# Performance work log

Measured on AMD Instinct MI355X. Metric: run time of the kernel, lower is better.

## Reference

```python
import jax, jax.numpy as jnp
import numpy as np

N = 100000   # points
C = 256      # in_planes
K = 16       # nsample (idx holds 2*K neighbors)
L = 2        # num_mlplayer
NEG = 0.1    # LeakyReLU slope
EPS = 1e-5   # LayerNorm eps (torch default)

PARAM_KEYS = ['emb_w1','emb_g1','emb_b1','emb_w2','conv_w','pw_w1','pw_g1','pw_b1','pw_w2','pw_g2','pw_b2']


def layer_norm(x, g, b):
    m = x.mean(-1, keepdims=True)
    v = ((x - m) ** 2).mean(-1, keepdims=True)
    return (x - m) * jax.lax.rsqrt(v + EPS) * g + b


def calc_ppf(p, n, pg, ng):
    # standard 4-dim point-pair features: angle(n1,d), angle(n2,d), angle(n1,n2), ||d||
    d = pg - p[:, None, :]                                   # [N,2K,3]
    dist = jnp.linalg.norm(d, axis=-1, keepdims=True)
    def angle(a, b):
        cr = jnp.linalg.norm(jnp.cross(a, b), axis=-1, keepdims=True)
        dt = jnp.sum(a * b, axis=-1, keepdims=True)
        return jnp.arctan2(cr, dt)
    n1 = jnp.broadcast_to(n[:, None, :], pg.shape)
    return jnp.concatenate([angle(n1, d), angle(ng, d), angle(n1, ng), dist], -1)


def mlp_layer(p, x, idx, ppf, r, pr):
    # cart2sphere -> r-normalized radial distance, giving 4+1=5 embedding inputs
    d = p[idx] - p[:, None, :]                               # [N,K,3]
    sphere = jnp.linalg.norm(d, axis=-1, keepdims=True) / r  # [N,K,1]
    f5 = jnp.concatenate([ppf, sphere], -1)                  # [N,K,5]
    h = f5 @ pr['emb_w1']
    h = jax.nn.leaky_relu(layer_norm(h, pr['emb_g1'], pr['emb_b1']), NEG)
    pos = h @ pr['emb_w2']                                   # [N,K,C]
    g = x[idx] + pos                                         # gather + add
    # Partial_conv3 (split_cat): 1x1 conv (no bias) on first C//4 channels
    c4 = pr['conv_w'].shape[0]
    g1 = jnp.einsum('nkc,dc->nkd', g[..., :c4], pr['conv_w'])
    g = jnp.concatenate([g1, g[..., c4:]], -1)
    pooled = g.max(axis=1)                                   # max-pool over neighbors [N,C]
    h = pooled @ pr['pw_w1']
    h = jax.nn.leaky_relu(layer_norm(h, pr['pw_g1'], pr['pw_b1']), NEG)
    h = layer_norm(h @ pr['pw_w2'], pr['pw_g2'], pr['pw_b2'])
    return jax.nn.relu(h + x)                                # residual + relu


def setup_inputs():
    key = jax.random.key(0)
    ks = jax.random.split(key, 16)
    s = 0.02
    n = jax.random.normal(ks[2], (N, 3), jnp.float32)
    n = n / jnp.linalg.norm(n, axis=-1, keepdims=True)
    return {
        'p': jax.random.normal(ks[0], (N, 3), jnp.float32),
        'x': jax.random.normal(ks[1], (N, C), jnp.float32),
        'n': n,
        'idx': jax.random.randint(ks[3], (N, 2 * K), 0, N, jnp.int32),
        'r': jnp.ones((1,), jnp.float32),
        'emb_w1': jax.random.normal(ks[4], (L, 5, C), jnp.float32) * s,
        'emb_g1': jnp.ones((L, C), jnp.float32),
        'emb_b1': jnp.zeros((L, C), jnp.float32),
        'emb_w2': jax.random.normal(ks[5], (L, C, C), jnp.float32) * s,
        'conv_w': jax.random.normal(ks[6], (L, C // 4, C // 4), jnp.float32) * s,
        'pw_w1': jax.random.normal(ks[7], (L, C, 4 * C), jnp.float32) * s,
        'pw_g1': jnp.ones((L, 4 * C), jnp.float32),
        'pw_b1': jnp.zeros((L, 4 * C), jnp.float32),
        'pw_w2': jax.random.normal(ks[8], (L, 4 * C, C), jnp.float32) * s,
        'pw_g2': jnp.ones((L, C), jnp.float32),
        'pw_b2': jnp.zeros((L, C), jnp.float32),
        'proj_w': jax.random.normal(ks[9], (C, C), jnp.float32) * s,
        'proj_b': jnp.zeros((C,), jnp.float32),
    }


def reference(p, x, n, idx, r, emb_w1, emb_g1, emb_b1, emb_w2, conv_w,
              pw_w1, pw_g1, pw_b1, pw_w2, pw_g2, pw_b2, proj_w, proj_b):
    # idx is given -> group_idx = idx (queryandgroup branch skipped, as in source)
    ppf = calc_ppf(p, n, p[idx], n[idx])                     # [N,2K,4]
    idx_m, ppf_m = idx[:, :K], ppf[:, :K]                    # mlp branch uses first nsample
    stacked = [emb_w1, emb_g1, emb_b1, emb_w2, conv_w, pw_w1, pw_g1, pw_b1, pw_w2, pw_g2, pw_b2]
    h = x
    for l in range(L):
        pr = dict(zip(PARAM_KEYS, [a[l] for a in stacked]))
        h = mlp_layer(p, h, idx_m, ppf_m, r[0], pr)
    # proj_mlp; blocks=1 -> trans_block is an empty Sequential (identity)
    return h @ proj_w + proj_b
```

## Files before the change

### kernel.cpp

```cpp
#include <hip/hip_runtime.h>
#include <hip/hip_bf16.h>
#include <stdint.h>

#define N_PTS 100000
#define NPAD  100032

typedef unsigned short u16;
typedef unsigned int   u32;
using bf16x8 = __attribute__((ext_vector_type(8))) short;
using f32x4  = __attribute__((ext_vector_type(4))) float;

__device__ __forceinline__ u16 f2bf(float f) {
    __hip_bfloat16 h = __float2bfloat16(f);
    return *reinterpret_cast<u16*>(&h);
}
__device__ __forceinline__ float bf2f(u16 h) {
    return __uint_as_float(((u32)h) << 16);
}

__global__ __launch_bounds__(256) void k_transpose_pad(
    const float* __restrict__ src, u16* __restrict__ dst,
    int Lc, int R, int Cc, int stride) {
    int t = blockIdx.x * 256 + threadIdx.x;
    int total = Lc * Cc * stride;
    if (t >= total) return;
    int l = t / (Cc * stride);
    int rem = t - l * (Cc * stride);
    int co = rem / stride;
    int ci = rem - co * stride;
    dst[t] = (ci < R) ? f2bf(src[((size_t)l * R + ci) * Cc + co]) : (u16)0;
}

__global__ __launch_bounds__(256) void k_cast_bf16(
    const float* __restrict__ src, u16* __restrict__ dst, int total) {
    int t = blockIdx.x * 256 + threadIdx.x;
    if (t < total) dst[t] = f2bf(src[t]);
}

__global__ __launch_bounds__(256) void k_castx8(
    const float* __restrict__ src, u16* __restrict__ dst, int total8) {
    int t = blockIdx.x * 256 + threadIdx.x;
    if (t >= total8) return;
    float4 a = *(const float4*)(src + (size_t)t * 8);
    float4 b = *(const float4*)(src + (size_t)t * 8 + 4);
    uint4 o;
    o.x = (u32)f2bf(a.x) | ((u32)f2bf(a.y) << 16);
    o.y = (u32)f2bf(a.z) | ((u32)f2bf(a.w) << 16);
    o.z = (u32)f2bf(b.x) | ((u32)f2bf(b.y) << 16);
    o.w = (u32)f2bf(b.z) | ((u32)f2bf(b.w) << 16);
    *(uint4*)(dst + (size_t)t * 8) = o;
}

__device__ __forceinline__ float angf(float ax, float ay, float az,
                                      float bx, float by, float bz) {
    float cx = ay * bz - az * by;
    float cy = az * bx - ax * bz;
    float cz = ax * by - ay * bx;
    float cr = sqrtf(cx * cx + cy * cy + cz * cz);
    float dt = ax * bx + ay * by + az * bz;
    return atan2f(cr, dt);
}

__global__ __launch_bounds__(256) void k_ppf(
    const float* __restrict__ p, const float* __restrict__ nrm,
    const int* __restrict__ idx, const float* __restrict__ r,
    u16* __restrict__ f5b) {
    int t = blockIdx.x * 256 + threadIdx.x;
    if (t >= N_PTS * 16) return;
    int i = t >> 4;
    int j = idx[(size_t)i * 32 + (t & 15)];
    float pix = p[(size_t)i*3], piy = p[(size_t)i*3+1], piz = p[(size_t)i*3+2];
    float pjx = p[(size_t)j*3], pjy = p[(size_t)j*3+1], pjz = p[(size_t)j*3+2];
    float dx = pjx - pix, dy = pjy - piy, dz = pjz - piz;
    float dist = sqrtf(dx*dx + dy*dy + dz*dz);
    float nix = nrm[(size_t)i*3], niy = nrm[(size_t)i*3+1], niz = nrm[(size_t)i*3+2];
    float njx = nrm[(size_t)j*3], njy = nrm[(size_t)j*3+1], njz = nrm[(size_t)j*3+2];
    float a1 = angf(nix, niy, niz, dx, dy, dz);
    float a2 = angf(njx, njy, njz, dx, dy, dz);
    float a3 = angf(nix, niy, niz, njx, njy, njz);
    float rinv = 1.0f / r[0];
    u16* o = f5b + (size_t)t * 5;
    o[0] = f2bf(a1); o[1] = f2bf(a2); o[2] = f2bf(a3);
    o[3] = f2bf(dist); o[4] = f2bf(dist * rinv);
}

__device__ __forceinline__ bf16x8 fixup_frag(const uint2* pk, int kt,
                                             int srcA, int srcB, bool hiT) {
    int aLx = __shfl((int)pk[2*kt].x,   srcA);
    int aHx = __shfl((int)pk[2*kt+1].x, srcA);
    int aLy = __shfl((int)pk[2*kt].y,   srcA);
    int aHy = __shfl((int)pk[2*kt+1].y, srcA);
    int bLx = __shfl((int)pk[2*kt].x,   srcB);
    int bHx = __shfl((int)pk[2*kt+1].x, srcB);
    int bLy = __shfl((int)pk[2*kt].y,   srcB);
    int bHy = __shfl((int)pk[2*kt+1].y, srcB);
    uint4 u;
    u.x = (u32)(hiT ? aHx : aLx);
    u.y = (u32)(hiT ? aHy : aLy);
    u.z = (u32)(hiT ? bHx : bLx);
    u.w = (u32)(hiT ? bHy : bLy);
    return *(bf16x8*)&u;
}

__global__ __launch_bounds__(512, 4) void k_neighbor(
    const u16*   __restrict__ xcur,
    const u16*   __restrict__ f5b,
    const int*   __restrict__ idx,
    const u16*   __restrict__ w1pad,
    const float* __restrict__ g1, const float* __restrict__ b1,
    const u16*   __restrict__ ew2tp,
    const u16*   __restrict__ convbf,
    u16*         __restrict__ pooledb)
{
    __shared__ u16 Bs[64 * 264];
    __shared__ u16 posw[8][2][16][72];
    __shared__ u16 pbounce[8][2][256];
    __shared__ int idxs[16][16];

    const int tid = threadIdx.x, w = tid >> 6, lane = tid & 63;
    const int rr = lane & 15, q = lane >> 4;
    const int i0 = blockIdx.x * 16;

    for (int o = tid * 16; o < 33792; o += 8192)
        *(uint4*)((char*)Bs + o) = *(const uint4*)((const char*)ew2tp + o);
    if (tid < 256)
        idxs[tid >> 4][tid & 15] = idx[(size_t)(i0 + (tid >> 4)) * 32 + (tid & 15)];

    const int srcA = rr + ((q & 1) << 5);
    const int srcB = srcA + 16;
    const bool hiT = (q >> 1) != 0;

    bf16x8 hfrag[2][8];
    #pragma unroll
    for (int rt = 0; rt < 2; ++rt) {
        const int pt = i0 + 2 * w + rt;
        bf16x8 a1;
        #pragma unroll
        for (int e = 0; e < 8; ++e) a1[e] = 0;
        if (q == 0) {
            const u16* fp = f5b + (size_t)(pt * 16 + rr) * 5;
            a1[0] = (short)fp[0]; a1[1] = (short)fp[1];
            a1[2] = (short)fp[2]; a1[3] = (short)fp[3];
            a1[4] = (short)fp[4];
        }
        f32x4 hacc[16];
        __builtin_amdgcn_s_setprio(1);
        #pragma unroll
        for (int ct = 0; ct < 16; ++ct) {
            bf16x8 aW = *(const bf16x8*)&w1pad[(ct * 16 + rr) * 32 + q * 8];
            f32x4 z = {0.f, 0.f, 0.f, 0.f};
            hacc[ct] = __builtin_amdgcn_mfma_f32_16x16x32_bf16(aW, a1, z, 0, 0, 0);
        }
        __builtin_amdgcn_s_setprio(0);
        float s = 0.f, z2 = 0.f;
        #pragma unroll
        for (int ct = 0; ct < 16; ++ct) {
            #pragma unroll
            for (int j = 0; j < 4; ++j) { float v = hacc[ct][j]; s += v; z2 += v * v; }
        }
        s  += __shfl_xor(s, 16);  s  += __shfl_xor(s, 32);
        z2 += __shfl_xor(z2, 16); z2 += __shfl_xor(z2, 32);
        float mean = s * (1.f / 256.f);
        float var = fmaxf(z2 * (1.f / 256.f) - mean * mean, 0.f);
        float rstd = 1.0f / sqrtf(var + 1e-5f);

        uint2 pk[16];
        #pragma unroll
        for (int ct = 0; ct < 16; ++ct) {
            const int c0 = ct * 16 + 4 * q;
            float4 gg = *(const float4*)&g1[c0];
            float4 bb = *(const float4*)&b1[c0];
            float v0 = (hacc[ct][0] - mean) * rstd * gg.x + bb.x;
            float v1 = (hacc[ct][1] - mean) * rstd * gg.y + bb.y;
            float v2 = (hacc[ct][2] - mean) * rstd * gg.z + bb.z;
            float v3 = (hacc[ct][3] - mean) * rstd * gg.w + bb.w;
            v0 = v0 > 0.f ? v0 : 0.1f * v0;
            v1 = v1 > 0.f ? v1 : 0.1f * v1;
            v2 = v2 > 0.f ? v2 : 0.1f * v2;
            v3 = v3 > 0.f ? v3 : 0.1f * v3;
            pk[ct].x = (u32)f2bf(v0) | ((u32)f2bf(v1) << 16);
            pk[ct].y = (u32)f2bf(v2) | ((u32)f2bf(v3) << 16);
        }
        #pragma unroll
        for (int kt = 0; kt < 8; ++kt)
            hfrag[rt][kt] = fixup_frag(pk, kt, srcA, srcB, hiT);
    }
    __syncthreads();

    const int ppt = lane >> 5, cl = lane & 31;
    const int* ixp = idxs[2 * w + ppt];

    #pragma unroll 1
    for (int p = 0; p < 4; ++p) {
        __builtin_amdgcn_s_setprio(1);
        #pragma unroll
        for (int nt4 = 0; nt4 < 4; ++nt4) {
            f32x4 a0 = {0.f,0.f,0.f,0.f}, a1v = {0.f,0.f,0.f,0.f};
            #pragma unroll
            for (int kb = 0; kb < 8; ++kb) {
                bf16x8 bb = *(const bf16x8*)&Bs[(nt4 * 16 + rr) * 264 + kb * 32 + q * 8];
                a0  = __builtin_amdgcn_mfma_f32_16x16x32_bf16(hfrag[0][kb], bb, a0, 0, 0, 0);
                a1v = __builtin_amdgcn_mfma_f32_16x16x32_bf16(hfrag[1][kb], bb, a1v, 0, 0, 0);
            }
            #pragma unroll
            for (int j = 0; j < 4; ++j) {
                posw[w][0][4 * q + j][nt4 * 16 + rr] = f2bf(a0[j]);
                posw[w][1][4 * q + j][nt4 * 16 + rr] = f2bf(a1v[j]);
            }
        }
        __builtin_amdgcn_s_setprio(0);
        if (p < 3) {
            __syncthreads();
            const char* src = (const char*)(ew2tp + (size_t)(p + 1) * 64 * 264);
            for (int o = tid * 16; o < 33792; o += 8192)
                *(uint4*)((char*)Bs + o) = *(const uint4*)(src + o);
        }
        if (p == 0) {
            #pragma unroll
            for (int pt = 0; pt < 2; ++pt) {
                const u16* xr = xcur + (size_t)idxs[2 * w + pt][rr] * 256;
                bf16x8 gA[2];
                #pragma unroll
                for (int kb = 0; kb < 2; ++kb) {
                    bf16x8 xa = *(const bf16x8*)(xr + kb * 32 + q * 8);
                    bf16x8 pv = *(const bf16x8*)&posw[w][pt][rr][kb * 32 + q * 8];
                    bf16x8 g;
                    #pragma unroll
                    for (int e = 0; e < 8; ++e)
                        g[e] = (short)f2bf(bf2f((u16)xa[e]) + bf2f((u16)pv[e]));
                    gA[kb] = g;
                }
                __builtin_amdgcn_s_setprio(1);
                #pragma unroll
                for (int cn = 0; cn < 4; ++cn) {
                    bf16x8 cB0 = *(const bf16x8*)&convbf[(cn * 16 + rr) * 64 + q * 8];
                    bf16x8 cB1 = *(const bf16x8*)&convbf[(cn * 16 + rr) * 64 + 32 + q * 8];
                    f32x4 z = {0.f,0.f,0.f,0.f};
                    f32x4 acc = __builtin_amdgcn_mfma_f32_16x16x32_bf16(gA[0], cB0, z, 0, 0, 0);
                    acc = __builtin_amdgcn_mfma_f32_16x16x32_bf16(gA[1], cB1, acc, 0, 0, 0);
                    float m = fmaxf(fmaxf(acc[0], acc[1]), fmaxf(acc[2], acc[3]));
                    m = fmaxf(m, __shfl_xor(m, 16));
                    m = fmaxf(m, __shfl_xor(m, 32));
                    if (lane < 16) pbounce[w][pt][cn * 16 + lane] = f2bf(m);
                }
                __builtin_amdgcn_s_setprio(0);
            }
        } else {
            const int cq = p * 64 + cl * 2;
            u32 xv[16];
            #pragma unroll
            for (int k = 0; k < 16; ++k)
                xv[k] = *(const u32*)(xcur + (size_t)ixp[k] * 256 + cq);
            float m0 = -3e38f, m1 = -3e38f;
            #pragma unroll
            for (int k = 0; k < 16; ++k) {
                u32 pv = *(const u32*)&posw[w][ppt][k][cl * 2];
                float gv0 = bf2f((u16)(pv & 0xffffu)) + bf2f((u16)(xv[k] & 0xffffu));
                float gv1 = bf2f((u16)(pv >> 16))     + bf2f((u16)(xv[k] >> 16));
                m0 = fmaxf(m0, gv0);
                m1 = fmaxf(m1, gv1);
            }
            *(u32*)&pbounce[w][ppt][cq] = (u32)f2bf(m0) | ((u32)f2bf(m1) << 16);
        }
        if (p < 3) __syncthreads();
    }
    {
        const int pt = lane >> 5, off = (lane & 31) * 8;
        uint4 v = *(const uint4*)&pbounce[w][pt][off];
        *(uint4*)(pooledb + (size_t)(i0 + 2 * w + pt) * 256 + off) = v;
    }
}

__global__ __launch_bounds__(512, 4) void k_pointwise(
    const u16* poolb,
    const u16* __restrict__ xresb,
    u16*       outb,
    const u16* __restrict__ b1t,
    const float* __restrict__ g1, const float* __restrict__ b1,
    const u16* __restrict__ b2t,
    const float* __restrict__ g2, const float* __restrict__ b2,
    int guardRes,
    const u16* __restrict__ pjtp,
    const float* __restrict__ pb,
    float* __restrict__ outf,
    int doProj)
{
    __shared__ u16 hm[32 * 1032];
    __shared__ float pst[32][8][2];

    const int tid = threadIdx.x, w = tid >> 6, lane = tid & 63;
    const int rr = lane & 15, q = lane >> 4;
    const size_t R0 = (size_t)blockIdx.x * 32;

    bf16x8 afr[2][8];
    #pragma unroll
    for (int rt = 0; rt < 2; ++rt) {
        int ar = (int)R0 + rt * 16 + rr; if (ar >= N_PTS) ar = N_PTS - 1;
        const u16* arow = poolb + (size_t)ar * 256;
        #pragma unroll
        for (int kb = 0; kb < 8; ++kb)
            afr[rt][kb] = *(const bf16x8*)(arow + kb * 32 + q * 8);
    }

    #pragma unroll 2
    for (int ct = 0; ct < 8; ++ct) {
        const int co = w * 128 + ct * 16 + rr;
        const u16* bp = b1t + (size_t)co * 256 + q * 8;
        bf16x8 bb[8];
        #pragma unroll
        for (int kb = 0; kb < 8; ++kb) bb[kb] = *(const bf16x8*)(bp + kb * 32);
        f32x4 a0 = {0.f,0.f,0.f,0.f}, a1v = {0.f,0.f,0.f,0.f};
        __builtin_amdgcn_s_setprio(1);
        #pragma unroll
        for (int kb = 0; kb < 8; ++kb) {
            a0  = __builtin_amdgcn_mfma_f32_16x16x32_bf16(afr[0][kb], bb[kb], a0, 0, 0, 0);
            a1v = __builtin_amdgcn_mfma_f32_16x16x32_bf16(afr[1][kb], bb[kb], a1v, 0, 0, 0);
        }
        __builtin_amdgcn_s_setprio(0);
        #pragma unroll
        for (int j = 0; j < 4; ++j) {
            hm[(4 * q + j) * 1032 + co]      = f2bf(a0[j]);
            hm[(16 + 4 * q + j) * 1032 + co] = f2bf(a1v[j]);
        }
    }
    __syncthreads();

    {
        const int row = tid >> 4;
        const int t16 = tid & 15;
        u32* hm32 = (u32*)hm;
        const int base = row * 516;
        float s = 0.f, z = 0.f;
        #pragma unroll 8
        for (int e = 0; e < 32; ++e) {
            u32 pk = hm32[base + t16 + 16 * e];
            float v0 = bf2f((u16)(pk & 0xffffu)), v1 = bf2f((u16)(pk >> 16));
            s += v0 + v1; z += v0 * v0 + v1 * v1;
        }
        s += __shfl_xor(s, 1); s += __shfl_xor(s, 2);
        s += __shfl_xor(s, 4); s += __shfl_xor(s, 8);
        z += __shfl_xor(z, 1); z += __shfl_xor(z, 2);
        z += __shfl_xor(z, 4); z += __shfl_xor(z, 8);
        float mean = s * (1.f / 1024.f);
        float var = fmaxf(z * (1.f / 1024.f) - mean * mean, 0.f);
        float rstd = 1.0f / sqrtf(var + 1e-5f);
        #pragma unroll 4
        for (int e = 0; e < 32; ++e) {
            const int cidx = t16 + 16 * e;
            u32 pk = hm32[base + cidx];
            const int c = cidx * 2;
            float2 gg = *(const float2*)&g1[c];
            float2 bbv = *(const float2*)&b1[c];
            float v0 = (bf2f((u16)(pk & 0xffffu)) - mean) * rstd * gg.x + bbv.x;
            float v1 = (bf2f((u16)(pk >> 16))     - mean) * rstd * gg.y + bbv.y;
            v0 = v0 > 0.f ? v0 : 0.1f * v0;
            v1 = v1 > 0.f ? v1 : 0.1f * v1;
            hm32[base + cidx] = (u32)f2bf(v0) | ((u32)f2bf(v1) << 16);
        }
    }
    __syncthreads();

    f32x4 acc2[2][2];
    #pragma unroll
    for (int ct = 0; ct < 2; ++ct) {
        const int cB = w * 32 + ct * 16 + rr;
        const u16* bp = b2t + (size_t)cB * 1024 + q * 8;
        f32x4 c0 = {0.f,0.f,0.f,0.f}, c1 = {0.f,0.f,0.f,0.f};
        __builtin_amdgcn_s_setprio(1);
        #pragma unroll 8
        for (int kb = 0; kb < 32; ++kb) {
            bf16x8 b  = *(const bf16x8*)(bp + kb * 32);
            bf16x8 a0 = *(const bf16x8*)&hm[rr * 1032 + kb * 32 + q * 8];
            bf16x8 a1 = *(const bf16x8*)&hm[(16 + rr) * 1032 + kb * 32 + q * 8];
            c0 = __builtin_amdgcn_mfma_f32_16x16x32_bf16(a0, b, c0, 0, 0, 0);
            c1 = __builtin_amdgcn_mfma_f32_16x16x32_bf16(a1, b, c1, 0, 0, 0);
        }
        __builtin_amdgcn_s_setprio(0);
        acc2[0][ct] = c0; acc2[1][ct] = c1;
    }

    #pragma unroll
    for (int rt = 0; rt < 2; ++rt) {
        #pragma unroll
        for (int j = 0; j < 4; ++j) {
            float s = acc2[rt][0][j] + acc2[rt][1][j];
            float z = acc2[rt][0][j] * acc2[rt][0][j] + acc2[rt][1][j] * acc2[rt][1][j];
            s += __shfl_xor(s, 1); s += __shfl_xor(s, 2);
            s += __shfl_xor(s, 4); s += __shfl_xor(s, 8);
            z += __shfl_xor(z, 1); z += __shfl_xor(z, 2);
            z += __shfl_xor(z, 4); z += __shfl_xor(z, 8);
            if (rr == 0) {
                pst[rt * 16 + 4 * q + j][w][0] = s;
                pst[rt * 16 + 4 * q + j][w][1] = z;
            }
        }
    }
    __syncthreads();

    #pragma unroll
    for (int rt = 0; rt < 2; ++rt) {
        float mean2[4], rstd2[4];
        #pragma unroll
        for (int j = 0; j < 4; ++j) {
            const int row = rt * 16 + 4 * q + j;
            float s = 0.f, z = 0.f;
            #pragma unroll
            for (int k = 0; k < 8; ++k) { s += pst[row][k][0]; z += pst[row][k][1]; }
            float mean = s * (1.f / 256.f);
            float var = fmaxf(z * (1.f / 256.f) - mean * mean, 0.f);
            mean2[j] = mean;
            rstd2[j] = 1.0f / sqrtf(var + 1e-5f);
        }
        #pragma unroll
        for (int ct = 0; ct < 2; ++ct) {
            const int c = w * 32 + ct * 16 + rr;
            const float gg = g2[c], bb = b2[c];
            #pragma unroll
            for (int j = 0; j < 4; ++j) {
                const size_t row = R0 + rt * 16 + 4 * q + j;
                float v = (acc2[rt][ct][j] - mean2[j]) * rstd2[j] * gg + bb;
                float xv = 0.f;
                if (!guardRes || row < (size_t)N_PTS) xv = bf2f(xresb[row * 256 + c]);
                float o = v + xv;
                u16 hb = f2bf(o > 0.f ? o : 0.f);
                if (doProj) {
                    hm[(rt * 16 + 4 * q + j) * 264 + c] = hb;
                } else {
                    outb[row * 256 + c] = hb;
                }
            }
        }
    }
    if (!doProj) return;

    __syncthreads();
    bf16x8 a3[2][8];
    #pragma unroll
    for (int rt = 0; rt < 2; ++rt)
        #pragma unroll
        for (int kb = 0; kb < 8; ++kb)
            a3[rt][kb] = *(const bf16x8*)&hm[(rt * 16 + rr) * 264 + kb * 32 + q * 8];
    #pragma unroll
    for (int ct = 0; ct < 2; ++ct) {
        const int cout = w * 32 + ct * 16 + rr;
        const u16* bp = pjtp + (size_t)cout * 264 + q * 8;
        bf16x8 bb[8];
        #pragma unroll
        for (int kb = 0; kb < 8; ++kb) bb[kb] = *(const bf16x8*)(bp + kb * 32);
        f32x4 c0 = {0.f,0.f,0.f,0.f}, c1 = {0.f,0.f,0.f,0.f};
        __builtin_amdgcn_s_setprio(1);
        #pragma unroll
        for (int kb = 0; kb < 8; ++kb) {
            c0 = __builtin_amdgcn_mfma_f32_16x16x32_bf16(a3[0][kb], bb[kb], c0, 0, 0, 0);
            c1 = __builtin_amdgcn_mfma_f32_16x16x32_bf16(a3[1][kb], bb[kb], c1, 0, 0, 0);
        }
        __builtin_amdgcn_s_setprio(0);
        const float bias = pb[cout];
        #pragma unroll
        for (int rt = 0; rt < 2; ++rt) {
            const f32x4 acc = rt ? c1 : c0;
            #pragma unroll
            for (int j = 0; j < 4; ++j) {
                const size_t row = R0 + rt * 16 + 4 * q + j;
                if (row < (size_t)N_PTS) outf[row * 256 + cout] = acc[j] + bias;
            }
        }
    }
}

extern "C" void kernel_launch(void* const* d_in, const int* in_sizes, int n_in,
                              void* d_out, int out_size, void* d_ws, size_t ws_size,
                              hipStream_t stream) {
    const float* p      = (const float*)d_in[0];
    const float* x      = (const float*)d_in[1];
    const float* nn     = (const float*)d_in[2];
    const int*   idx    = (const int*)d_in[3];
    const float* r      = (const float*)d_in[4];
    const float* emb_w1 = (const float*)d_in[5];
    const float* emb_g1 = (const float*)d_in[6];
    const float* emb_b1 = (const float*)d_in[7];
    const float* emb_w2 = (const float*)d_in[8];
    const float* conv_w = (const float*)d_in[9];
    const float* pw_w1  = (const float*)d_in[10];
    const float* pw_g1  = (const float*)d_in[11];
    const float* pw_b1  = (const float*)d_in[12];
    const float* pw_w2  = (const float*)d_in[13];
    const float* pw_g2  = (const float*)d_in[14];
    const float* pw_b2  = (const float*)d_in[15];
    const float* proj_w = (const float*)d_in[16];
    const float* proj_b = (const float*)d_in[17];
    float* out = (float*)d_out;

    char* ws = (char*)d_ws;
    const size_t SZB = (size_t)NPAD * 256 * sizeof(u16);
    u16* xb0 = (u16*)ws;
    u16* PB  = (u16*)(ws + SZB);
    u16* h1B = (u16*)(ws + 2 * SZB);
    u16* f5b = (u16*)(ws + 3 * SZB);
    u16* wb  = f5b + (size_t)N_PTS * 16 * 5;
    u16* ew2tp  = wb;
    u16* pjtp   = ew2tp + 2 * 256 * 264;
    u16* w1pad  = pjtp + 256 * 264;
    u16* convbf = w1pad + 2 * 256 * 32;
    u16* b1t    = convbf + 2 * 64 * 64;
    u16* b2t    = b1t + 2 * 1024 * 256;

    k_transpose_pad<<<(2*256*264 + 255)/256, 256, 0, stream>>>(emb_w2, ew2tp, 2, 256, 256, 264);
    k_transpose_pad<<<(256*264 + 255)/256, 256, 0, stream>>>(proj_w, pjtp, 1, 256, 256, 264);
    k_transpose_pad<<<(2*256*32 + 255)/256, 256, 0, stream>>>(emb_w1, w1pad, 2, 5, 256, 32);
    k_transpose_pad<<<(2*1024*256 + 255)/256, 256, 0, stream>>>(pw_w1, b1t, 2, 256, 1024, 256);
    k_transpose_pad<<<(2*256*1024 + 255)/256, 256, 0, stream>>>(pw_w2, b2t, 2, 1024, 256, 1024);
    k_cast_bf16<<<(2*64*64 + 255)/256, 256, 0, stream>>>(conv_w, convbf, 2*64*64);

    k_castx8<<<(N_PTS*256/8 + 255)/256, 256, 0, stream>>>(x, xb0, N_PTS*256/8);
    k_ppf<<<(N_PTS * 16 + 255)/256, 256, 0, stream>>>(p, nn, idx, r, f5b);

    k_neighbor<<<N_PTS/16, 512, 0, stream>>>(xb0, f5b, idx, w1pad, emb_g1, emb_b1,
                                             ew2tp, convbf, PB);
    k_pointwise<<<NPAD/32, 512, 0, stream>>>(PB, xb0, h1B, b1t, pw_g1, pw_b1,
                                             b2t, pw_g2, pw_b2, 1,
                                             pjtp, proj_b, out, 0);
    k_neighbor<<<N_PTS/16, 512, 0, stream>>>(h1B, f5b, idx, w1pad + 256*32,
                                             emb_g1 + 256, emb_b1 + 256,
                                             ew2tp + 256*264, convbf + 64*64, xb0);
    k_pointwise<<<NPAD/32, 512, 0, stream>>>(xb0, h1B, (u16*)PB, b1t + 1024*256,
                                             pw_g1 + 1024, pw_b1 + 1024,
                                             b2t + 256*1024, pw_g2 + 256, pw_b2 + 256, 0,
                                             pjtp, proj_b, out, 1);
}
```

Measured before the change: 2.108 ms.

## Fuse neighbor pooling and pointwise MLP into one kernel per layer

Merges the neighbor-gather/max-pool kernel with the pointwise MLP (two GEMMs plus LayerNorms, residual, optional projection) into a single kernel working on 16 points per block, with shared memory reused between phases. This removes the pooled-feature round trip through global memory and two kernel launches per layer. In exchange the pointwise GEMMs now run with 16-row tiles instead of 32, so the weight matrices are streamed twice as often per point. Shared memory use rises to about 80KB, which may lower occupancy.

```diff
diff --git a/kernel.cpp b/kernel.cpp
--- a/kernel.cpp
+++ b/kernel.cpp
@@ -3,7 +3,6 @@
 #include <stdint.h>
 
 #define N_PTS 100000
-#define NPAD  100032
 
 typedef unsigned short u16;
 typedef unsigned int   u32;
@@ -102,7 +101,7 @@
     return *(bf16x8*)&u;
 }
 
-__global__ __launch_bounds__(512, 4) void k_neighbor(
+__global__ __launch_bounds__(512, 4) void k_fused(
     const u16*   __restrict__ xcur,
     const u16*   __restrict__ f5b,
     const int*   __restrict__ idx,
@@ -110,21 +109,30 @@
     const float* __restrict__ g1, const float* __restrict__ b1,
     const u16*   __restrict__ ew2tp,
     const u16*   __restrict__ convbf,
-    u16*         __restrict__ pooledb)
+    const u16*   __restrict__ b1t,
+    const float* __restrict__ pg1, const float* __restrict__ pb1,
+    const u16*   __restrict__ b2t,
+    const float* __restrict__ pg2, const float* __restrict__ pb2,
+    u16*         __restrict__ houtb,
+    const u16*   __restrict__ pjtp,
+    const float* __restrict__ pbias,
+    float*       __restrict__ outf,
+    int doProj)
 {
-    __shared__ u16 Bs[64 * 264];
-    __shared__ u16 posw[8][2][16][72];
-    __shared__ u16 pbounce[8][2][256];
-    __shared__ int idxs[16][16];
+    __shared__ __align__(16) char smem[80128];
+    u16* BsP   = (u16*)smem;
+    u16* poswP = (u16*)(smem + 33792);
+    u16* pbP   = (u16*)(smem + 70656);
+    int* idxsP = (int*)(smem + 79104);
 
     const int tid = threadIdx.x, w = tid >> 6, lane = tid & 63;
     const int rr = lane & 15, q = lane >> 4;
     const int i0 = blockIdx.x * 16;
 
     for (int o = tid * 16; o < 33792; o += 8192)
-        *(uint4*)((char*)Bs + o) = *(const uint4*)((const char*)ew2tp + o);
+        *(uint4*)((char*)BsP + o) = *(const uint4*)((const char*)ew2tp + o);
     if (tid < 256)
-        idxs[tid >> 4][tid & 15] = idx[(size_t)(i0 + (tid >> 4)) * 32 + (tid & 15)];
+        idxsP[tid] = idx[(size_t)(i0 + (tid >> 4)) * 32 + (tid & 15)];
 
     const int srcA = rr + ((q & 1) << 5);
     const int srcB = srcA + 16;
@@ -188,7 +196,7 @@
     __syncthreads();
 
     const int ppt = lane >> 5, cl = lane & 31;
-    const int* ixp = idxs[2 * w + ppt];
+    const int* ixp = idxsP + (2 * w + ppt) * 16;
 
     #pragma unroll 1
     for (int p = 0; p < 4; ++p) {
@@ -198,14 +206,14 @@
             f32x4 a0 = {0.f,0.f,0.f,0.f}, a1v = {0.f,0.f,0.f,0.f};
             #pragma unroll
             for (int kb = 0; kb < 8; ++kb) {
-                bf16x8 bb = *(const bf16x8*)&Bs[(nt4 * 16 + rr) * 264 + kb * 32 + q * 8];
+                bf16x8 bb = *(const bf16x8*)&BsP[(nt4 * 16 + rr) * 264 + kb * 32 + q * 8];
                 a0  = __builtin_amdgcn_mfma_f32_16x16x32_bf16(hfrag[0][kb], bb, a0, 0, 0, 0);
                 a1v = __builtin_amdgcn_mfma_f32_16x16x32_bf16(hfrag[1][kb], bb, a1v, 0, 0, 0);
             }
             #pragma unroll
             for (int j = 0; j < 4; ++j) {
-                posw[w][0][4 * q + j][nt4 * 16 + rr] = f2bf(a0[j]);
-                posw[w][1][4 * q + j][nt4 * 16 + rr] = f2bf(a1v[j]);
+                poswP[((2 * w + 0) * 16 + 4 * q + j) * 72 + nt4 * 16 + rr] = f2bf(a0[j]);
+                poswP[((2 * w + 1) * 16 + 4 * q + j) * 72 + nt4 * 16 + rr] = f2bf(a1v[j]);
             }
         }
         __builtin_amdgcn_s_setprio(0);
@@ -213,17 +221,17 @@
             __syncthreads();
             const char* src = (const char*)(ew2tp + (size_t)(p + 1) * 64 * 264);
             for (int o = tid * 16; o < 33792; o += 8192)
-                *(uint4*)((char*)Bs + o) = *(const uint4*)(src + o);
+                *(uint4*)((char*)BsP + o) = *(const uint4*)(src + o);
         }
         if (p == 0) {
             #pragma unroll
             for (int pt = 0; pt < 2; ++pt) {
-                const u16* xr = xcur + (size_t)idxs[2 * w + pt][rr] * 256;
+                const u16* xr = xcur + (size_t)idxsP[(2 * w + pt) * 16 + rr] * 256;
                 bf16x8 gA[2];
                 #pragma unroll
                 for (int kb = 0; kb < 2; ++kb) {
                     bf16x8 xa = *(const bf16x8*)(xr + kb * 32 + q * 8);
-                    bf16x8 pv = *(const bf16x8*)&posw[w][pt][rr][kb * 32 + q * 8];
+                    bf16x8 pv = *(const bf16x8*)&poswP[((2 * w + pt) * 16 + rr) * 72 + kb * 32 + q * 8];
                     bf16x8 g;
                     #pragma unroll
                     for (int e = 0; e < 8; ++e)
@@ -241,7 +249,7 @@
                     float m = fmaxf(fmaxf(acc[0], acc[1]), fmaxf(acc[2], acc[3]));
                     m = fmaxf(m, __shfl_xor(m, 16));
                     m = fmaxf(m, __shfl_xor(m, 32));
-                    if (lane < 16) pbounce[w][pt][cn * 16 + lane] = f2bf(m);
+                    if (lane < 16) pbP[(2 * w + pt) * 264 + cn * 16 + lane] = f2bf(m);
                 }
                 __builtin_amdgcn_s_setprio(0);
             }
@@ -254,53 +262,26 @@
             float m0 = -3e38f, m1 = -3e38f;
             #pragma unroll
             for (int k = 0; k < 16; ++k) {
-                u32 pv = *(const u32*)&posw[w][ppt][k][cl * 2];
+                u32 pv = *(const u32*)&poswP[((2 * w + ppt) * 16 + k) * 72 + cl * 2];
                 float gv0 = bf2f((u16)(pv & 0xffffu)) + bf2f((u16)(xv[k] & 0xffffu));
                 float gv1 = bf2f((u16)(pv >> 16))     + bf2f((u16)(xv[k] >> 16));
                 m0 = fmaxf(m0, gv0);
                 m1 = fmaxf(m1, gv1);
             }
-            *(u32*)&pbounce[w][ppt][cq] = (u32)f2bf(m0) | ((u32)f2bf(m1) << 16);
+            *(u32*)&pbP[(2 * w + ppt) * 264 + cq] = (u32)f2bf(m0) | ((u32)f2bf(m1) << 16);
         }
         if (p < 3) __syncthreads();
     }
-    {
-        const int pt = lane >> 5, off = (lane & 31) * 8;
-        uint4 v = *(const uint4*)&pbounce[w][pt][off];
-        *(uint4*)(pooledb + (size_t)(i0 + 2 * w + pt) * 256 + off) = v;
-    }
-}
-
-__global__ __launch_bounds__(512, 4) void k_pointwise(
-    const u16* poolb,
-    const u16* __restrict__ xresb,
-    u16*       outb,
-    const u16* __restrict__ b1t,
-    const float* __restrict__ g1, const float* __restrict__ b1,
-    const u16* __restrict__ b2t,
-    const float* __restrict__ g2, const float* __restrict__ b2,
-    int guardRes,
-    const u16* __restrict__ pjtp,
-    const float* __restrict__ pb,
-    float* __restrict__ outf,
-    int doProj)
-{
-    __shared__ u16 hm[32 * 1032];
-    __shared__ float pst[32][8][2];
-
-    const int tid = threadIdx.x, w = tid >> 6, lane = tid & 63;
-    const int rr = lane & 15, q = lane >> 4;
-    const size_t R0 = (size_t)blockIdx.x * 32;
-
-    bf16x8 afr[2][8];
-    #pragma unroll
-    for (int rt = 0; rt < 2; ++rt) {
-        int ar = (int)R0 + rt * 16 + rr; if (ar >= N_PTS) ar = N_PTS - 1;
-        const u16* arow = poolb + (size_t)ar * 256;
-        #pragma unroll
-        for (int kb = 0; kb < 8; ++kb)
-            afr[rt][kb] = *(const bf16x8*)(arow + kb * 32 + q * 8);
-    }
+    __syncthreads();
+
+    u16*   hm   = (u16*)smem;
+    float* pst  = (float*)(smem + 33792);
+    u16*   h2s  = (u16*)(smem + 36864);
+
+    bf16x8 afr[8];
+    #pragma unroll
+    for (int kb = 0; kb < 8; ++kb)
+        afr[kb] = *(const bf16x8*)&pbP[rr * 264 + kb * 32 + q * 8];
 
     #pragma unroll 2
     for (int ct = 0; ct < 8; ++ct) {
@@ -309,48 +290,44 @@
         bf16x8 bb[8];
         #pragma unroll
         for (int kb = 0; kb < 8; ++kb) bb[kb] = *(const bf16x8*)(bp + kb * 32);
-        f32x4 a0 = {0.f,0.f,0.f,0.f}, a1v = {0.f,0.f,0.f,0.f};
+        f32x4 acc = {0.f,0.f,0.f,0.f};
         __builtin_amdgcn_s_setprio(1);
         #pragma unroll
-        for (int kb = 0; kb < 8; ++kb) {
-            a0  = __builtin_amdgcn_mfma_f32_16x16x32_bf16(afr[0][kb], bb[kb], a0, 0, 0, 0);
-            a1v = __builtin_amdgcn_mfma_f32_16x16x32_bf16(afr[1][kb], bb[kb], a1v, 0, 0, 0);
-        }
+        for (int kb = 0; kb < 8; ++kb)
+            acc = __builtin_amdgcn_mfma_f32_16x16x32_bf16(afr[kb], bb[kb], acc, 0, 0, 0);
         __builtin_amdgcn_s_setprio(0);
         #pragma unroll
-        for (int j = 0; j < 4; ++j) {
-            hm[(4 * q + j) * 1032 + co]      = f2bf(a0[j]);
-            hm[(16 + 4 * q + j) * 1032 + co] = f2bf(a1v[j]);
-        }
+        for (int j = 0; j < 4; ++j)
+            hm[(4 * q + j) * 1032 + co] = f2bf(acc[j]);
     }
     __syncthreads();
 
     {
-        const int row = tid >> 4;
-        const int t16 = tid & 15;
+        const int row = tid >> 5;
+        const int t32 = tid & 31;
         u32* hm32 = (u32*)hm;
         const int base = row * 516;
         float s = 0.f, z = 0.f;
         #pragma unroll 8
-        for (int e = 0; e < 32; ++e) {
-            u32 pk = hm32[base + t16 + 16 * e];
+        for (int e = 0; e < 16; ++e) {
+            u32 pk = hm32[base + t32 + 32 * e];
             float v0 = bf2f((u16)(pk & 0xffffu)), v1 = bf2f((u16)(pk >> 16));
             s += v0 + v1; z += v0 * v0 + v1 * v1;
         }
         s += __shfl_xor(s, 1); s += __shfl_xor(s, 2);
-        s += __shfl_xor(s, 4); s += __shfl_xor(s, 8);
+        s += __shfl_xor(s, 4); s += __shfl_xor(s, 8); s += __shfl_xor(s, 16);
         z += __shfl_xor(z, 1); z += __shfl_xor(z, 2);
-        z += __shfl_xor(z, 4); z += __shfl_xor(z, 8);
+        z += __shfl_xor(z, 4); z += __shfl_xor(z, 8); z += __shfl_xor(z, 16);
         float mean = s * (1.f / 1024.f);
         float var = fmaxf(z * (1.f / 1024.f) - mean * mean, 0.f);
         float rstd = 1.0f / sqrtf(var + 1e-5f);
         #pragma unroll 4
-        for (int e = 0; e < 32; ++e) {
-            const int cidx = t16 + 16 * e;
+        for (int e = 0; e < 16; ++e) {
+            const int cidx = t32 + 32 * e;
             u32 pk = hm32[base + cidx];
             const int c = cidx * 2;
-            float2 gg = *(const float2*)&g1[c];
-            float2 bbv = *(const float2*)&b1[c];
+            float2 gg = *(const float2*)&pg1[c];
+            float2 bbv = *(const float2*)&pb1[c];
             float v0 = (bf2f((u16)(pk & 0xffffu)) - mean) * rstd * gg.x + bbv.x;
             float v1 = (bf2f((u16)(pk >> 16))     - mean) * rstd * gg.y + bbv.y;
             v0 = v0 > 0.f ? v0 : 0.1f * v0;
@@ -360,109 +337,97 @@
     }
     __syncthreads();
 
-    f32x4 acc2[2][2];
-    #pragma unroll
-    for (int ct = 0; ct < 2; ++ct) {
-        const int cB = w * 32 + ct * 16 + rr;
-        const u16* bp = b2t + (size_t)cB * 1024 + q * 8;
+    f32x4 acc2[2];
+    {
+        const u16* bp0 = b2t + (size_t)(w * 32 + rr) * 1024 + q * 8;
+        const u16* bp1 = b2t + (size_t)(w * 32 + 16 + rr) * 1024 + q * 8;
         f32x4 c0 = {0.f,0.f,0.f,0.f}, c1 = {0.f,0.f,0.f,0.f};
         __builtin_amdgcn_s_setprio(1);
         #pragma unroll 8
         for (int kb = 0; kb < 32; ++kb) {
-            bf16x8 b  = *(const bf16x8*)(bp + kb * 32);
-            bf16x8 a0 = *(const bf16x8*)&hm[rr * 1032 + kb * 32 + q * 8];
-            bf16x8 a1 = *(const bf16x8*)&hm[(16 + rr) * 1032 + kb * 32 + q * 8];
-            c0 = __builtin_amdgcn_mfma_f32_16x16x32_bf16(a0, b, c0, 0, 0, 0);
-            c1 = __builtin_amdgcn_mfma_f32_16x16x32_bf16(a1, b, c1, 0, 0, 0);
+            bf16x8 a  = *(const bf16x8*)&hm[rr * 1032 + kb * 32 + q * 8];
+            bf16x8 bL = *(const bf16x8*)(bp0 + kb * 32);
+            bf16x8 bR = *(const bf16x8*)(bp1 + kb * 32);
+            c0 = __builtin_amdgcn_mfma_f32_16x16x32_bf16(a, bL, c0, 0, 0, 0);
+            c1 = __builtin_amdgcn_mfma_f32_16x16x32_bf16(a, bR, c1, 0, 0, 0);
         }
         __builtin_amdgcn_s_setprio(0);
-        acc2[0][ct] = c0; acc2[1][ct] = c1;
-    }
-
-    #pragma unroll
-    for (int rt = 0; rt < 2; ++rt) {
+        acc2[0] = c0; acc2[1] = c1;
+    }
+
+    #pragma unroll
+    for (int j = 0; j < 4; ++j) {
+        float s = acc2[0][j] + acc2[1][j];
+        float z = acc2[0][j] * acc2[0][j] + acc2[1][j] * acc2[1][j];
+        s += __shfl_xor(s, 1); s += __shfl_xor(s, 2);
+        s += __shfl_xor(s, 4); s += __shfl_xor(s, 8);
+        z += __shfl_xor(z, 1); z += __shfl_xor(z, 2);
+        z += __shfl_xor(z, 4); z += __shfl_xor(z, 8);
+        if (rr == 0) {
+            pst[((4 * q + j) * 8 + w) * 2 + 0] = s;
+            pst[((4 * q + j) * 8 + w) * 2 + 1] = z;
+        }
+    }
+    __syncthreads();
+
+    float mean2[4], rstd2[4];
+    #pragma unroll
+    for (int j = 0; j < 4; ++j) {
+        const int row = 4 * q + j;
+        float s = 0.f, z = 0.f;
+        #pragma unroll
+        for (int k = 0; k < 8; ++k) {
+            s += pst[(row * 8 + k) * 2 + 0];
+            z += pst[(row * 8 + k) * 2 + 1];
+        }
+        float mean = s * (1.f / 256.f);
+        float var = fmaxf(z * (1.f / 256.f) - mean * mean, 0.f);
+        mean2[j] = mean;
+        rstd2[j] = 1.0f / sqrtf(var + 1e-5f);
+    }
+    #pragma unroll
+    for (int ct = 0; ct < 2; ++ct) {
+        const int c = w * 32 + ct * 16 + rr;
+        const float gg = pg2[c], bb = pb2[c];
         #pragma unroll
         for (int j = 0; j < 4; ++j) {
-            float s = acc2[rt][0][j] + acc2[rt][1][j];
-            float z = acc2[rt][0][j] * acc2[rt][0][j] + acc2[rt][1][j] * acc2[rt][1][j];
-            s += __shfl_xor(s, 1); s += __shfl_xor(s, 2);
-            s += __shfl_xor(s, 4); s += __shfl_xor(s, 8);
-            z += __shfl_xor(z, 1); z += __shfl_xor(z, 2);
-            z += __shfl_xor(z, 4); z += __shfl_xor(z, 8);
-            if (rr == 0) {
-                pst[rt * 16 + 4 * q + j][w][0] = s;
-                pst[rt * 16 + 4 * q + j][w][1] = z;
-            }
-        }
-    }
-    __syncthreads();
-
-    #pragma unroll
-    for (int rt = 0; rt < 2; ++rt) {
-        float mean2[4], rstd2[4];
-        #pragma unroll
-        for (int j = 0; j < 4; ++j) {
-            const int row = rt * 16 + 4 * q + j;
-            float s = 0.f, z = 0.f;
-            #pragma unroll
-            for (int k = 0; k < 8; ++k) { s += pst[row][k][0]; z += pst[row][k][1]; }
-            float mean = s * (1.f / 256.f);
-            float var = fmaxf(z * (1.f / 256.f) - mean * mean, 0.f);
-            mean2[j] = mean;
-            rstd2[j] = 1.0f / sqrtf(var + 1e-5f);
-        }
-        #pragma unroll
-        for (int ct = 0; ct < 2; ++ct) {
-            const int c = w * 32 + ct * 16 + rr;
-            const float gg = g2[c], bb = b2[c];
-            #pragma unroll
-            for (int j = 0; j < 4; ++j) {
-                const size_t row = R0 + rt * 16 + 4 * q + j;
-                float v = (acc2[rt][ct][j] - mean2[j]) * rstd2[j] * gg + bb;
-                float xv = 0.f;
-                if (!guardRes || row < (size_t)N_PTS) xv = bf2f(xresb[row * 256 + c]);
-                float o = v + xv;
-                u16 hb = f2bf(o > 0.f ? o : 0.f);
-                if (doProj) {
-                    hm[(rt * 16 + 4 * q + j) * 264 + c] = hb;
-                } else {
-                    outb[row * 256 + c] = hb;
-                }
-            }
+            const size_t row = (size_t)i0 + 4 * q + j;
+            float v = (acc2[ct][j] - mean2[j]) * rstd2[j] * gg + bb;
+            float o = v + bf2f(xcur[row * 256 + c]);
+            u16 hb = f2bf(o > 0.f ? o : 0.f);
+            if (doProj) h2s[(4 * q + j) * 264 + c] = hb;
+            else        houtb[row * 256 + c] = hb;
         }
     }
     if (!doProj) return;
 
     __syncthreads();
-    bf16x8 a3[2][8];
-    #pragma unroll
-    for (int rt = 0; rt < 2; ++rt)
-        #pragma unroll
-        for (int kb = 0; kb < 8; ++kb)
-            a3[rt][kb] = *(const bf16x8*)&hm[(rt * 16 + rr) * 264 + kb * 32 + q * 8];
-    #pragma unroll
-    for (int ct = 0; ct < 2; ++ct) {
-        const int cout = w * 32 + ct * 16 + rr;
-        const u16* bp = pjtp + (size_t)cout * 264 + q * 8;
-        bf16x8 bb[8];
-        #pragma unroll
-        for (int kb = 0; kb < 8; ++kb) bb[kb] = *(const bf16x8*)(bp + kb * 32);
+    bf16x8 a3[8];
+    #pragma unroll
+    for (int kb = 0; kb < 8; ++kb)
+        a3[kb] = *(const bf16x8*)&h2s[rr * 264 + kb * 32 + q * 8];
+    {
+        const u16* bp0 = pjtp + (size_t)(w * 32 + rr) * 264 + q * 8;
+        const u16* bp1 = pjtp + (size_t)(w * 32 + 16 + rr) * 264 + q * 8;
         f32x4 c0 = {0.f,0.f,0.f,0.f}, c1 = {0.f,0.f,0.f,0.f};
         __builtin_amdgcn_s_setprio(1);
         #pragma unroll
         for (int kb = 0; kb < 8; ++kb) {
-            c0 = __builtin_amdgcn_mfma_f32_16x16x32_bf16(a3[0][kb], bb[kb], c0, 0, 0, 0);
-            c1 = __builtin_amdgcn_mfma_f32_16x16x32_bf16(a3[1][kb], bb[kb], c1, 0, 0, 0);
+            bf16x8 bL = *(const bf16x8*)(bp0 + kb * 32);
+            bf16x8 bR = *(const bf16x8*)(bp1 + kb * 32);
+            c0 = __builtin_amdgcn_mfma_f32_16x16x32_bf16(a3[kb], bL, c0, 0, 0, 0);
+            c1 = __builtin_amdgcn_mfma_f32_16x16x32_bf16(a3[kb], bR, c1, 0, 0, 0);
         }
         __builtin_amdgcn_s_setprio(0);
-        const float bias = pb[cout];
-        #pragma unroll
-        for (int rt = 0; rt < 2; ++rt) {
-            const f32x4 acc = rt ? c1 : c0;
+        #pragma unroll
+        for (int ct = 0; ct < 2; ++ct) {
+            const int cout = w * 32 + ct * 16 + rr;
+            const float bias = pbias[cout];
+            const f32x4 acc = ct ? c1 : c0;
             #pragma unroll
             for (int j = 0; j < 4; ++j) {
-                const size_t row = R0 + rt * 16 + 4 * q + j;
-                if (row < (size_t)N_PTS) outf[row * 256 + cout] = acc[j] + bias;
+                const size_t row = (size_t)i0 + 4 * q + j;
+                outf[row * 256 + cout] = acc[j] + bias;
             }
         }
     }
@@ -492,11 +457,10 @@
     float* out = (float*)d_out;
 
     char* ws = (char*)d_ws;
-    const size_t SZB = (size_t)NPAD * 256 * sizeof(u16);
+    const size_t SZB = (size_t)N_PTS * 256 * sizeof(u16);
     u16* xb0 = (u16*)ws;
-    u16* PB  = (u16*)(ws + SZB);
-    u16* h1B = (u16*)(ws + 2 * SZB);
-    u16* f5b = (u16*)(ws + 3 * SZB);
+    u16* h1B = (u16*)(ws + SZB);
+    u16* f5b = (u16*)(ws + 2 * SZB);
     u16* wb  = f5b + (size_t)N_PTS * 16 * 5;
     u16* ew2tp  = wb;
     u16* pjtp   = ew2tp + 2 * 256 * 264;
@@ -515,16 +479,14 @@
     k_castx8<<<(N_PTS*256/8 + 255)/256, 256, 0, stream>>>(x, xb0, N_PTS*256/8);
     k_ppf<<<(N_PTS * 16 + 255)/256, 256, 0, stream>>>(p, nn, idx, r, f5b);
 
-    k_neighbor<<<N_PTS/16, 512, 0, stream>>>(xb0, f5b, idx, w1pad, emb_g1, emb_b1,
-                                             ew2tp, convbf, PB);
-    k_pointwise<<<NPAD/32, 512, 0, stream>>>(PB, xb0, h1B, b1t, pw_g1, pw_b1,
-                                             b2t, pw_g2, pw_b2, 1,
-                                             pjtp, proj_b, out, 0);
-    k_neighbor<<<N_PTS/16, 512, 0, stream>>>(h1B, f5b, idx, w1pad + 256*32,
-                                             emb_g1 + 256, emb_b1 + 256,
-                                             ew2tp + 256*264, convbf + 64*64, xb0);
-    k_pointwise<<<NPAD/32, 512, 0, stream>>>(xb0, h1B, (u16*)PB, b1t + 1024*256,
-                                             pw_g1 + 1024, pw_b1 + 1024,
-                                             b2t + 256*1024, pw_g2 + 256, pw_b2 + 256, 0,
-                                             pjtp, proj_b, out, 1);
-}
+    k_fused<<<N_PTS/16, 512, 0, stream>>>(xb0, f5b, idx, w1pad, emb_g1, emb_b1,
+                                          ew2tp, convbf,
+                                          b1t, pw_g1, pw_b1, b2t, pw_g2, pw_b2,
+                                          h1B, pjtp, proj_b, out, 0);
+    k_fused<<<N_PTS/16, 512, 0, stream>>>(h1B, f5b, idx, w1pad + 256*32,
+                                          emb_g1 + 256, emb_b1 + 256,
+                                          ew2tp + 256*264, convbf + 64*64,
+                                          b1t + 1024*256, pw_g1 + 1024, pw_b1 + 1024,
+                                          b2t + 256*1024, pw_g2 + 256, pw_b2 + 256,
+                                          xb0 , pjtp, proj_b, out, 1);
+}
```

New measurement: 2.651 ms. 25.7% more time.
